# Optimization experiments

Measured on AMD Instinct MI355X. Metric: run time of the kernel, lower is better.

## Reference

```python
import jax, jax.numpy as jnp
import numpy as np

IN_CH = 512
STYLE_DIM = 512
K_ATT = 4  # block size used in forward()


def make_up_kernel():
    # make_kernel([1,3,3,1]) -> outer product, normalized; Upsample scales by factor**2
    k = jnp.array([1.0, 3.0, 3.0, 1.0], jnp.float32)
    k = k[None, :] * k[:, None]
    k = k / k.sum()
    return k * 4.0  # factor**2 with factor=2


def setup_inputs() -> dict:
    key = jax.random.key(0)
    ks = jax.random.split(key, 8)
    B, H, W = 8, 128, 128
    return {
        "input": jax.random.normal(ks[0], (B, IN_CH, H, W), jnp.float32),
        "style": jax.random.normal(ks[1], (B, STYLE_DIM), jnp.float32),
        "skip": jax.random.normal(ks[2], (B, 3, H // 2, W // 2), jnp.float32),
        "attention0": jax.random.normal(ks[3], (B, 3, H, W), jnp.float32),
        "attention1": jax.random.normal(ks[4], (B, 3, H, W), jnp.float32),
        # learned params
        "conv_w": jax.random.normal(ks[5], (3, IN_CH), jnp.float32),  # ModulatedConv2d weight (1x1 kernel squeezed)
        "mod_w": jax.random.normal(ks[6], (IN_CH, STYLE_DIM), jnp.float32),  # EqualLinear weight
        "mod_b": jnp.ones((IN_CH,), jnp.float32),  # bias_init=1
        "bias": jnp.zeros((1, 3, 1, 1), jnp.float32),
        "q_w": jax.random.normal(ks[7], (1, 3, 3, 3), jnp.float32) * 0.1,  # query_conv weight [O=1,I=3,3,3]
        "q_b": jnp.zeros((1,), jnp.float32),
        "up_kernel": make_up_kernel(),  # registered buffer
    }


def _upsample2x(x, kernel):
    # upfirdn2d(x, kernel, up=2, pad=(2,1)); kernel is symmetric so flip is a no-op.
    # lhs_dilation=2 inserts zeros between samples (length 2H-1); torch's upfirdn also
    # appends one trailing zero, so the right pad becomes pad1+1 = 2.
    C = x.shape[1]
    k = jnp.broadcast_to(kernel[None, None], (C, 1, 4, 4))
    return jax.lax.conv_general_dilated(
        x, k, window_strides=(1, 1), padding=((2, 2), (2, 2)),
        lhs_dilation=(2, 2), feature_group_count=C)


def _conv3x3(x, w, b):
    out = jax.lax.conv_general_dilated(x, w, (1, 1), ((1, 1), (1, 1)))
    return out + b[None, :, None, None]


def _blockify(x, k):
    # F.unfold(x, k, stride=k) for single-channel x: [B,1,H,W] -> [B, k*k, (H/k)*(W/k)]
    B, _, H, W = x.shape
    x = x.reshape(B, H // k, k, W // k, k)
    return x.transpose(0, 2, 4, 1, 3).reshape(B, k * k, (H // k) * (W // k))


def _unblockify(u, k, H, W):
    # F.fold inverse (non-overlapping): [B, k*k, L] -> [B,1,H,W]
    B = u.shape[0]
    x = u.reshape(B, k, k, H // k, W // k)
    return x.transpose(0, 3, 1, 4, 2).reshape(B, 1, H, W)


def _l2norm(u, axes):
    return u / jnp.maximum(jnp.sqrt(jnp.sum(u * u, axis=axes, keepdims=True)), 1e-12)


def reference(input, style, skip, attention0, attention1,
              conv_w, mod_w, mod_b, bias, q_w, q_b, up_kernel):
    B, Cin, H, W = input.shape
    # EqualLinear modulation: scale = 1/sqrt(style_dim)
    s = style @ (mod_w * (1.0 / np.sqrt(STYLE_DIM))).T + mod_b  # [B, Cin]
    # ModulatedConv2d, kernel_size=1, demodulate=False, group=batch conv -> per-sample scaled 1x1 conv
    conv_scale = 1.0 / np.sqrt(Cin)  # fan_in = in_channel * 1**2
    out = jnp.einsum('oi,bi,bihw->bohw', conv_w * conv_scale, s, input) + bias

    # skip path
    skip_up = _upsample2x(skip, up_kernel)

    # attention map (width > k branch, k=4)
    k = K_ATT
    pq = _conv3x3(jax.lax.stop_gradient(attention0), q_w, q_b)  # [B,1,H,W]
    pk = _conv3x3(jax.lax.stop_gradient(attention1), q_w, q_b)
    qu = _l2norm(_blockify(pq, k), axes=1)  # [B, k*k, L], L2 per column (dim=1)
    ku = _l2norm(_blockify(pk, k), axes=1)
    energy = qu * ku
    energy_star = _l2norm(energy, axes=(1, 2)) * k  # F.normalize over dims (1,2), scaled by k
    att = _unblockify(energy_star, k, H, W)  # [B,1,H,W]

    out = out * att + skip_up * (1.0 - att)
    return out
```

## Files before the change

kernel.cpp:

```cpp
#include <hip/hip_runtime.h>
#include <math.h>

#define HW 16384
#define K1CH 64
#define SLICE 7


__device__ __forceinline__ void conv_pair(const float* __restrict__ p0b,
                                          const float* __restrict__ p1b,
                                          const float* __restrict__ qw,
                                          float qb, int h, int w, float& pq,
                                          float& pk) {
  pq = qb;
  pk = qb;
#pragma unroll
  for (int ci = 0; ci < 3; ++ci) {
    const float* p0 = p0b + (size_t)ci * HW;
    const float* p1 = p1b + (size_t)ci * HW;
#pragma unroll
    for (int ky = 0; ky < 3; ++ky) {
      int hh = h + ky - 1;
      if ((unsigned)hh >= 128u) continue;
#pragma unroll
      for (int kx = 0; kx < 3; ++kx) {
        int ww = w + kx - 1;
        if ((unsigned)ww >= 128u) continue;
        float wq = qw[ci * 9 + ky * 3 + kx];
        pq = fmaf(wq, p0[hh * 128 + ww], pq);
        pk = fmaf(wq, p1[hh * 128 + ww], pk);
      }
    }
  }
}

__global__ __launch_bounds__(256) void k1(
    const float* __restrict__ input, const float* __restrict__ style,
    const float* __restrict__ a0in, const float* __restrict__ a1in,
    const float* __restrict__ conv_w, const float* __restrict__ mod_w,
    const float* __restrict__ mod_b, const float* __restrict__ q_w,
    const float* __restrict__ q_b, float* __restrict__ energy,
    float* __restrict__ part, float4* __restrict__ weffhi,
    float* __restrict__ outp) {
  __shared__ __align__(16) float st[512];
  __shared__ float4 wl[K1CH];
  __shared__ float qw[27];
  __shared__ float qb_sh;
  __shared__ float partl[4];

  int t = threadIdx.x;
  int blk = blockIdx.x;
  int b = blk >> 6, j = blk & 63;
  int p = j * 256 + t;

  const float* in = input + (size_t)b * 512 * HW + p;

  float va[32], vb[32];
#pragma unroll
  for (int u = 0; u < 32; ++u) va[u] = in[(size_t)u * HW];
#pragma unroll
  for (int u = 0; u < 32; ++u) vb[u] = in[(size_t)(32 + u) * HW];

  st[t] = style[b * 512 + t];
  st[t + 256] = style[b * 512 + 256 + t];
  if (t < 27) qw[t] = q_w[t];
  if (t == 27) qb_sh = q_b[0];
  __syncthreads();

  const float kInv = 0.04419417382415922f;

  {
    int c = t >> 2, q = t & 3;
    const float4* row =
        reinterpret_cast<const float4*>(mod_w + (size_t)c * 512) + q * 32;
    const float4* sv = reinterpret_cast<const float4*>(st) + q * 32;
    float s = 0.f;
#pragma unroll
    for (int u = 0; u < 32; ++u) {
      float4 r = row[u];
      float4 sx = sv[u];
      s += r.x * sx.x + r.y * sx.y + r.z * sx.z + r.w * sx.w;
    }
    s += __shfl_xor(s, 1);
    s += __shfl_xor(s, 2);
    if (q == 0) {
      float sm = s * kInv + mod_b[c];
      wl[c] = make_float4(conv_w[c] * kInv * sm, conv_w[512 + c] * kInv * sm,
                          conv_w[1024 + c] * kInv * sm, 0.f);
    }
  }

  if (t < SLICE * 4) {
    int sI = t >> 2, q = t & 3;
    int c = K1CH + j * SLICE + sI;
    const float4* row =
        reinterpret_cast<const float4*>(mod_w + (size_t)c * 512) + q * 32;
    const float4* sv = reinterpret_cast<const float4*>(st) + q * 32;
    float s = 0.f;
#pragma unroll
    for (int u = 0; u < 32; ++u) {
      float4 r = row[u];
      float4 sx = sv[u];
      s += r.x * sx.x + r.y * sx.y + r.z * sx.z + r.w * sx.w;
    }
    s += __shfl_xor(s, 1);
    s += __shfl_xor(s, 2);
    if (q == 0) {
      float sm = s * kInv + mod_b[c];
      weffhi[(size_t)b * 448 + (c - K1CH)] =
          make_float4(conv_w[c] * kInv * sm, conv_w[512 + c] * kInv * sm,
                      conv_w[1024 + c] * kInv * sm, 0.f);
    }
  }

  {
    int by = j >> 1, bx = t >> 3, sub = t & 7;
    int hA = 4 * by + (sub >> 2), wA = 4 * bx + (sub & 3);
    const float* a0b = a0in + (size_t)(b * 3) * HW;
    const float* a1b = a1in + (size_t)(b * 3) * HW;
    float pq1, pk1, pq2, pk2;
    conv_pair(a0b, a1b, qw, qb_sh, hA, wA, pq1, pk1);
    conv_pair(a0b, a1b, qw, qb_sh, hA + 2, wA, pq2, pk2);

    float s_q = pq1 * pq1 + pq2 * pq2;
    float s_k = pk1 * pk1 + pk2 * pk2;
#pragma unroll
    for (int m = 1; m < 8; m <<= 1) {
      s_q += __shfl_xor(s_q, m);
      s_k += __shfl_xor(s_k, m);
    }
    float qn = 1.0f / fmaxf(sqrtf(s_q), 1e-12f);
    float kn = 1.0f / fmaxf(sqrtf(s_k), 1e-12f);
    float e1 = (pq1 * qn) * (pk1 * kn);
    float e2 = (pq2 * qn) * (pk2 * kn);

    float own = (j & 1) ? e2 : e1;
    energy[(size_t)b * HW + (2 * j + (sub >> 2)) * 128 + 4 * bx + (sub & 3)] =
        own;

    float ss = e1 * e1 + e2 * e2;
#pragma unroll
    for (int m = 1; m < 64; m <<= 1) ss += __shfl_xor(ss, m);
    int wid = t >> 6;
    if ((t & 63) == 0) partl[wid] = ss;
  }

  __syncthreads();
  if (t == 0 && (j & 1) == 0)
    part[b * 32 + (j >> 1)] = partl[0] + partl[1] + partl[2] + partl[3];

  float A0 = 0.f, A1 = 0.f, A2 = 0.f;
#pragma unroll
  for (int u = 0; u < 32; ++u) {
    float4 w = wl[u];
    A0 = fmaf(w.x, va[u], A0);
    A1 = fmaf(w.y, va[u], A1);
    A2 = fmaf(w.z, va[u], A2);
  }
#pragma unroll
  for (int u = 0; u < 32; ++u) {
    float4 w = wl[32 + u];
    A0 = fmaf(w.x, vb[u], A0);
    A1 = fmaf(w.y, vb[u], A1);
    A2 = fmaf(w.z, vb[u], A2);
  }
  size_t ob = (size_t)(b * 3) * HW + p;
  outp[ob] = A0;
  outp[ob + HW] = A1;
  outp[ob + 2 * HW] = A2;
}

__global__ __launch_bounds__(256) void k2(
    const float* __restrict__ input, const float4* __restrict__ weffhi,
    const float* __restrict__ bias, const float* __restrict__ skip,
    const float* __restrict__ upk, const float* __restrict__ energy,
    const float* __restrict__ part, float* __restrict__ outp) {
  __shared__ float4 lw[512];
  __shared__ float ssq_sh;
  int t = threadIdx.x;
  int blk = blockIdx.x;
  int b = blk >> 6, j = blk & 63;
  int p = j * 256 + t;

  const float4* g = weffhi + (size_t)b * 448;
  if (t < 224) {
    lw[64 + t] = g[t];
    lw[288 + t] = g[224 + t];
  }
  if (t < 32) {
    float ps = part[b * 32 + t];
#pragma unroll
    for (int m = 1; m < 32; m <<= 1) ps += __shfl_xor(ps, m);
    if (t == 0) ssq_sh = ps;
  }

  float e = energy[(size_t)b * HW + p];
  size_t ob = (size_t)(b * 3) * HW + p;
  float A0 = outp[ob], A1 = outp[ob + HW], A2 = outp[ob + 2 * HW];
  int y = p >> 7, x = p & 127;
  int syb = ((y + (y & 1)) >> 1) - 1;
  int sxb = ((x + (x & 1)) >> 1) - 1;
  int ky0 = y & 1, kx0 = x & 1;
  float sk0 = 0.f, sk1 = 0.f, sk2 = 0.f;
#pragma unroll
  for (int a = 0; a < 2; ++a) {
    int sy = syb + a;
    if ((unsigned)sy >= 64u) continue;
#pragma unroll
    for (int c2 = 0; c2 < 2; ++c2) {
      int sx = sxb + c2;
      if ((unsigned)sx >= 64u) continue;
      float kv = upk[(ky0 + 2 * a) * 4 + (kx0 + 2 * c2)];
      size_t base = ((size_t)(b * 3) * 64 + sy) * 64 + sx;
      sk0 = fmaf(kv, skip[base], sk0);
      sk1 = fmaf(kv, skip[base + 4096], sk1);
      sk2 = fmaf(kv, skip[base + 8192], sk2);
    }
  }
  float bi0 = bias[0], bi1 = bias[1], bi2 = bias[2];

  __syncthreads();

  const float* in = input + (size_t)b * 512 * HW + p;
  for (int c0 = 64; c0 < 512; c0 += 32) {
    float v[32];
#pragma unroll
    for (int u = 0; u < 32; ++u) v[u] = in[(size_t)(c0 + u) * HW];
#pragma unroll
    for (int u = 0; u < 32; ++u) {
      float4 w = lw[c0 + u];
      A0 = fmaf(w.x, v[u], A0);
      A1 = fmaf(w.y, v[u], A1);
      A2 = fmaf(w.z, v[u], A2);
    }
  }

  float att = e * (4.0f / fmaxf(sqrtf(ssq_sh), 1e-12f));
  float om = 1.0f - att;
  outp[ob] = (A0 + bi0) * att + sk0 * om;
  outp[ob + HW] = (A1 + bi1) * att + sk1 * om;
  outp[ob + 2 * HW] = (A2 + bi2) * att + sk2 * om;
}

extern "C" void kernel_launch(void* const* d_in, const int* in_sizes, int n_in,
                              void* d_out, int out_size, void* d_ws,
                              size_t ws_size, hipStream_t stream) {
  const float* input  = (const float*)d_in[0];
  const float* style  = (const float*)d_in[1];
  const float* skip   = (const float*)d_in[2];
  const float* att0   = (const float*)d_in[3];
  const float* att1   = (const float*)d_in[4];
  const float* conv_w = (const float*)d_in[5];
  const float* mod_w  = (const float*)d_in[6];
  const float* mod_b  = (const float*)d_in[7];
  const float* bias   = (const float*)d_in[8];
  const float* q_w    = (const float*)d_in[9];
  const float* q_b    = (const float*)d_in[10];
  const float* upk    = (const float*)d_in[11];

  int B = in_sizes[1] / 512;

  float* ws = (float*)d_ws;
  float* energy = ws;
  float* part   = ws + 131072;
  float4* weffhi = (float4*)(ws + 131072 + 256);
  float* outp = (float*)d_out;

  k1<<<B * 64, 256, 0, stream>>>(input, style, att0, att1, conv_w, mod_w,
                                 mod_b, q_w, q_b, energy, part, weffhi, outp);
  k2<<<B * 64, 256, 0, stream>>>(input, weffhi, bias, skip, upk, energy, part,
                                 outp);
}
```

Measured before the change: 70.14 us.

## Compute one attention pixel per thread and defer input channel loads in k1

The attention conv is remapped so each thread computes a single 3x3 conv output for one pixel of a 4x4 block, instead of two pixels with half the work discarded. The per-block partial sums are written per block (64 per batch) and k2 reduces over 64 entries, with the workspace offset for the effective weights moved to match. The 64-channel input loads in k1 are moved from the kernel start to after the attention computation, as a loop of register batches. This halves the redundant conv work but no longer overlaps the input loads with the style and attention computation.

```diff
diff --git a/kernel.cpp b/kernel.cpp
--- a/kernel.cpp
+++ b/kernel.cpp
@@ -5,33 +5,6 @@
 #define K1CH 64
 #define SLICE 7
 
-
-__device__ __forceinline__ void conv_pair(const float* __restrict__ p0b,
-                                          const float* __restrict__ p1b,
-                                          const float* __restrict__ qw,
-                                          float qb, int h, int w, float& pq,
-                                          float& pk) {
-  pq = qb;
-  pk = qb;
-#pragma unroll
-  for (int ci = 0; ci < 3; ++ci) {
-    const float* p0 = p0b + (size_t)ci * HW;
-    const float* p1 = p1b + (size_t)ci * HW;
-#pragma unroll
-    for (int ky = 0; ky < 3; ++ky) {
-      int hh = h + ky - 1;
-      if ((unsigned)hh >= 128u) continue;
-#pragma unroll
-      for (int kx = 0; kx < 3; ++kx) {
-        int ww = w + kx - 1;
-        if ((unsigned)ww >= 128u) continue;
-        float wq = qw[ci * 9 + ky * 3 + kx];
-        pq = fmaf(wq, p0[hh * 128 + ww], pq);
-        pk = fmaf(wq, p1[hh * 128 + ww], pk);
-      }
-    }
-  }
-}
 
 __global__ __launch_bounds__(256) void k1(
     const float* __restrict__ input, const float* __restrict__ style,
@@ -52,14 +25,6 @@
   int b = blk >> 6, j = blk & 63;
   int p = j * 256 + t;
 
-  const float* in = input + (size_t)b * 512 * HW + p;
-
-  float va[32], vb[32];
-#pragma unroll
-  for (int u = 0; u < 32; ++u) va[u] = in[(size_t)u * HW];
-#pragma unroll
-  for (int u = 0; u < 32; ++u) vb[u] = in[(size_t)(32 + u) * HW];
-
   st[t] = style[b * 512 + t];
   st[t + 256] = style[b * 512 + 256 + t];
   if (t < 27) qw[t] = q_w[t];
@@ -113,31 +78,44 @@
   }
 
   {
-    int by = j >> 1, bx = t >> 3, sub = t & 7;
-    int hA = 4 * by + (sub >> 2), wA = 4 * bx + (sub & 3);
-    const float* a0b = a0in + (size_t)(b * 3) * HW;
-    const float* a1b = a1in + (size_t)(b * 3) * HW;
-    float pq1, pk1, pq2, pk2;
-    conv_pair(a0b, a1b, qw, qb_sh, hA, wA, pq1, pk1);
-    conv_pair(a0b, a1b, qw, qb_sh, hA + 2, wA, pq2, pk2);
-
-    float s_q = pq1 * pq1 + pq2 * pq2;
-    float s_k = pk1 * pk1 + pk2 * pk2;
-#pragma unroll
-    for (int m = 1; m < 8; m <<= 1) {
-      s_q += __shfl_xor(s_q, m);
-      s_k += __shfl_xor(s_k, m);
-    }
-    float qn = 1.0f / fmaxf(sqrtf(s_q), 1e-12f);
-    float kn = 1.0f / fmaxf(sqrtf(s_k), 1e-12f);
-    float e1 = (pq1 * qn) * (pk1 * kn);
-    float e2 = (pq2 * qn) * (pk2 * kn);
-
-    float own = (j & 1) ? e2 : e1;
-    energy[(size_t)b * HW + (2 * j + (sub >> 2)) * 128 + 4 * bx + (sub & 3)] =
-        own;
-
-    float ss = e1 * e1 + e2 * e2;
+    int colLocal = t >> 4;
+    int pos = t & 15;
+    int col = j * 16 + colLocal;
+    int by = col >> 5, bx = col & 31;
+    int iy = pos >> 2, ix = pos & 3;
+    int h = by * 4 + iy, w = bx * 4 + ix;
+
+    float pq = qb_sh, pk = qb_sh;
+#pragma unroll
+    for (int ci = 0; ci < 3; ++ci) {
+      const float* p0 = a0in + (size_t)(b * 3 + ci) * HW;
+      const float* p1 = a1in + (size_t)(b * 3 + ci) * HW;
+#pragma unroll
+      for (int ky = 0; ky < 3; ++ky) {
+        int hh = h + ky - 1;
+        if ((unsigned)hh >= 128u) continue;
+#pragma unroll
+        for (int kx = 0; kx < 3; ++kx) {
+          int ww = w + kx - 1;
+          if ((unsigned)ww >= 128u) continue;
+          float wq = qw[ci * 9 + ky * 3 + kx];
+          pq = fmaf(wq, p0[hh * 128 + ww], pq);
+          pk = fmaf(wq, p1[hh * 128 + ww], pk);
+        }
+      }
+    }
+    float sq = pq * pq, sk = pk * pk;
+#pragma unroll
+    for (int m = 1; m < 16; m <<= 1) {
+      sq += __shfl_xor(sq, m);
+      sk += __shfl_xor(sk, m);
+    }
+    float qn = 1.0f / fmaxf(sqrtf(sq), 1e-12f);
+    float kn = 1.0f / fmaxf(sqrtf(sk), 1e-12f);
+    float e = (pq * qn) * (pk * kn);
+    energy[(size_t)b * HW + h * 128 + w] = e;
+
+    float ss = e * e;
 #pragma unroll
     for (int m = 1; m < 64; m <<= 1) ss += __shfl_xor(ss, m);
     int wid = t >> 6;
@@ -145,23 +123,21 @@
   }
 
   __syncthreads();
-  if (t == 0 && (j & 1) == 0)
-    part[b * 32 + (j >> 1)] = partl[0] + partl[1] + partl[2] + partl[3];
-
+  if (t == 0) part[blk] = partl[0] + partl[1] + partl[2] + partl[3];
+
+  const float* in = input + (size_t)b * 512 * HW + p;
   float A0 = 0.f, A1 = 0.f, A2 = 0.f;
-#pragma unroll
-  for (int u = 0; u < 32; ++u) {
-    float4 w = wl[u];
-    A0 = fmaf(w.x, va[u], A0);
-    A1 = fmaf(w.y, va[u], A1);
-    A2 = fmaf(w.z, va[u], A2);
-  }
-#pragma unroll
-  for (int u = 0; u < 32; ++u) {
-    float4 w = wl[32 + u];
-    A0 = fmaf(w.x, vb[u], A0);
-    A1 = fmaf(w.y, vb[u], A1);
-    A2 = fmaf(w.z, vb[u], A2);
+  for (int c0 = 0; c0 < K1CH; c0 += 32) {
+    float v[32];
+#pragma unroll
+    for (int u = 0; u < 32; ++u) v[u] = in[(size_t)(c0 + u) * HW];
+#pragma unroll
+    for (int u = 0; u < 32; ++u) {
+      float4 w = wl[c0 + u];
+      A0 = fmaf(w.x, v[u], A0);
+      A1 = fmaf(w.y, v[u], A1);
+      A2 = fmaf(w.z, v[u], A2);
+    }
   }
   size_t ob = (size_t)(b * 3) * HW + p;
   outp[ob] = A0;
@@ -186,10 +162,10 @@
     lw[64 + t] = g[t];
     lw[288 + t] = g[224 + t];
   }
-  if (t < 32) {
-    float ps = part[b * 32 + t];
-#pragma unroll
-    for (int m = 1; m < 32; m <<= 1) ps += __shfl_xor(ps, m);
+  if (t < 64) {
+    float ps = part[b * 64 + t];
+#pragma unroll
+    for (int m = 1; m < 64; m <<= 1) ps += __shfl_xor(ps, m);
     if (t == 0) ssq_sh = ps;
   }
 
@@ -262,7 +238,7 @@
   float* ws = (float*)d_ws;
   float* energy = ws;
   float* part   = ws + 131072;
-  float4* weffhi = (float4*)(ws + 131072 + 256);
+  float4* weffhi = (float4*)(ws + 131072 + 512);
   float* outp = (float*)d_out;
 
   k1<<<B * 64, 256, 0, stream>>>(input, style, att0, att1, conv_w, mod_w,
```

Result: faster. 67.07 us (-4.4%).
